# Kernel tuning notes

Hardware: AMD Instinct MI355X
Metric: run time of the kernel (lower is better)

## Reference

```python
import jax, jax.numpy as jnp
import numpy as np

NEG_SLOPE = 0.2  # leaky_relu negative slope (alpha)

def _glorot(key, shape):
    fan_in, fan_out = shape[0], shape[-1]
    lim = jnp.sqrt(6.0 / (fan_in + fan_out))
    return jax.random.uniform(key, shape, jnp.float32, -lim, lim)

def setup_inputs() -> dict:
    key = jax.random.key(0)
    ks = jax.random.split(key, 10)
    N, E, F_IN, HID, HEADS, NCLASS = 50000, 800000, 512, 32, 8, 32
    x = jax.random.normal(ks[0], (N, F_IN), jnp.float32)
    edge_index = jax.random.randint(ks[1], (2, E), 0, N, jnp.int64)
    # layer 1: heads=8, out per head = 32, concat -> 256
    W1 = _glorot(ks[2], (F_IN, HEADS * HID))
    att_src1 = _glorot(ks[3], (HEADS, HID))
    att_dst1 = _glorot(ks[4], (HEADS, HID))
    b1 = jnp.zeros((HEADS * HID,), jnp.float32)
    # layer 2: heads=1, out = nclass
    W2 = _glorot(ks[5], (HEADS * HID, NCLASS))
    att_src2 = _glorot(ks[6], (1, NCLASS))
    att_dst2 = _glorot(ks[7], (1, NCLASS))
    b2 = jnp.zeros((NCLASS,), jnp.float32)
    return {"x": x, "edge_index": edge_index, "W1": W1, "att_src1": att_src1,
            "att_dst1": att_dst1, "b1": b1, "W2": W2, "att_src2": att_src2,
            "att_dst2": att_dst2, "b2": b2}

def gat_conv(x, src, dst, W, a_src, a_dst, bias, num_nodes):
    """PyG GATConv (eval mode, self loops already appended to src/dst)."""
    H, C = a_src.shape
    h = (x @ W).reshape(num_nodes, H, C)                 # [N,H,C]
    score_src = jnp.einsum('nhc,hc->nh', h, a_src)       # [N,H]
    score_dst = jnp.einsum('nhc,hc->nh', h, a_dst)       # [N,H]
    e = jax.nn.leaky_relu(score_src[src] + score_dst[dst], NEG_SLOPE)  # [E,H]
    m = jax.ops.segment_max(e, dst, num_segments=num_nodes)           # [N,H]
    w = jnp.exp(e - m[dst])
    denom = jax.ops.segment_sum(w, dst, num_segments=num_nodes)       # [N,H]
    alpha = w / (denom[dst] + 1e-16)                                  # [E,H]
    out = jax.ops.segment_sum(alpha[:, :, None] * h[src], dst,
                              num_segments=num_nodes)                 # [N,H,C]
    return out.reshape(num_nodes, H * C) + bias

def reference(x, edge_index, W1, att_src1, att_dst1, b1, W2, att_src2, att_dst2, b2):
    N = x.shape[0]
    loops = jnp.arange(N, dtype=edge_index.dtype)
    src = jnp.concatenate([edge_index[0], loops])  # PyG add_self_loops=True
    dst = jnp.concatenate([edge_index[1], loops])
    h = jax.nn.elu(gat_conv(x, src, dst, W1, att_src1, att_dst1, b1, N))
    out = gat_conv(h, src, dst, W2, att_src2, att_dst2, b2, N)
    return out + 1e-06
```

## Files before the change

### kernel.cpp

```cpp
#include <hip/hip_runtime.h>
#include <math.h>

#define N_NODES 50000
#define N_EDGES 800000
#define E2 (N_EDGES + N_NODES)
#define F_IN 512
#define HEADS 8
#define HID 32
#define HC 256
#define NCLASS 32
#define NEG_SLOPE 0.2f
#define ELLW 64

typedef unsigned int uint;
typedef unsigned short ushort;
typedef __attribute__((ext_vector_type(8))) short bf16x8;
typedef __attribute__((ext_vector_type(4))) float f32x4;

#define GLOBAL_LOAD_LDS16(g, l) \
    __builtin_amdgcn_global_load_lds((const __attribute__((address_space(1))) void*)(g), \
                                     (__attribute__((address_space(3))) void*)(l), 16, 0, 0)

__device__ inline uint bf16_rne_bits(float f) {
    uint u = __float_as_uint(f);
    return (u + 0x7fffu + ((u >> 16) & 1u)) >> 16;
}
__device__ inline float bf2f(ushort u) { return __uint_as_float(((uint)u) << 16); }

#define W1_BLOCKS 512
#define W2_BLOCKS 32
#define FILL_BLOCKS ((E2 / 4 + 255) / 256)

__global__ void __launch_bounds__(256) prep_kernel(const float* __restrict__ W1,
        ushort* __restrict__ w1hi, ushort* __restrict__ w1lo,
        const float* __restrict__ W2, ushort* __restrict__ w2hi, ushort* __restrict__ w2lo,
        const int* __restrict__ ei, int* __restrict__ cursor, int* __restrict__ ell) {
    int b = blockIdx.x;
    if (b < W1_BLOCKS) {
        int t = b * 256 + threadIdx.x;
        int n = t >> 9, k = t & 511;
        float f = W1[k * 256 + n];
        uint h = bf16_rne_bits(f);
        float r = f - __uint_as_float(h << 16);
        w1hi[t] = (ushort)h;
        w1lo[t] = (ushort)bf16_rne_bits(r);
    } else if (b < W1_BLOCKS + W2_BLOCKS) {
        int t = (b - W1_BLOCKS) * 256 + threadIdx.x;
        int n = t >> 8, k = t & 255;
        float f = W2[k * 32 + n];
        uint h = bf16_rne_bits(f);
        float r = f - __uint_as_float(h << 16);
        w2hi[t] = (ushort)h;
        w2lo[t] = (ushort)bf16_rne_bits(r);
    } else {
        int e0 = ((b - W1_BLOCKS - W2_BLOCKS) * 256 + threadIdx.x) * 4;
        if (e0 < E2) {
            int src[4], dst[4];
            if (e0 < N_EDGES) {
                int4 s4 = *(const int4*)(ei + e0);
                int4 d4 = *(const int4*)(ei + N_EDGES + e0);
                src[0] = s4.x; src[1] = s4.y; src[2] = s4.z; src[3] = s4.w;
                dst[0] = d4.x; dst[1] = d4.y; dst[2] = d4.z; dst[3] = d4.w;
            } else {
                #pragma unroll
                for (int j = 0; j < 4; ++j) { src[j] = e0 + j - N_EDGES; dst[j] = src[j]; }
            }
            #pragma unroll
            for (int j = 0; j < 4; ++j) {
                int d = dst[j];
                int p = atomicAdd(&cursor[d], 1);
                ell[d * ELLW + p] = src[j];
            }
        }
    }
}

__global__ void __launch_bounds__(256) gemm1_mfma_kernel(const uint* __restrict__ xp,
        const ushort* __restrict__ bhi,
        const float* __restrict__ as1, const float* __restrict__ ad1,
        ushort* __restrict__ C, float* __restrict__ ssrc, float* __restrict__ sdst, int M) {
    __shared__ uint   As[128 * 32];
    __shared__ ushort Bh[128 * 32];
    const int tid = threadIdx.x, lane = tid & 63, wave = tid >> 6;

    const int NW = ((N_NODES + 127) / 128) * 2;
    const int orig = blockIdx.y * gridDim.x + blockIdx.x;
    const int xcd = orig & 7, idx = orig >> 3;
    const int q = NW >> 3, r = NW & 7;
    const int nid = (xcd < r ? xcd * (q + 1) : r * (q + 1) + (xcd - r) * q) + idx;
    const int bm = (nid >> 1) * 128, bn = (nid & 1) * 128;

    const uint* agp[4]; const uint* alp[4];
    #pragma unroll
    for (int s = 0; s < 4; ++s) {
        int t = wave * 4 + s;
        int p = t * 64 + lane;
        int row = p >> 3, cs = p & 7;
        int c = cs ^ (row & 7);
        int grow = bm + row; if (grow > M - 1) grow = M - 1;
        agp[s] = xp + ((size_t)grow * 512 + c * 4);
        alp[s] = &As[t * 256];
    }
    const ushort* bhgp[2]; const ushort* bhlp[2];
    #pragma unroll
    for (int s = 0; s < 2; ++s) {
        int t = wave * 2 + s;
        int p = t * 64 + lane;
        int row = p >> 2, qs = p & 3;
        int qq = qs ^ ((row >> 1) & 3);
        size_t go = (size_t)(bn + row) * 512 + qq * 8;
        bhgp[s] = bhi + go;
        bhlp[s] = &Bh[t * 512];
    }

    f32x4 acc[4][4] = {};
    const int wm = (wave >> 1) * 64, wn = (wave & 1) * 64;
    const int fm = lane & 15, quad = lane >> 4;

    for (int kk = 0; kk < 16; ++kk) {
        #pragma unroll
        for (int s = 0; s < 4; ++s) GLOBAL_LOAD_LDS16(agp[s], alp[s]);
        #pragma unroll
        for (int s = 0; s < 2; ++s) GLOBAL_LOAD_LDS16(bhgp[s], bhlp[s]);
        #pragma unroll
        for (int s = 0; s < 4; ++s) agp[s] += 32;
        #pragma unroll
        for (int s = 0; s < 2; ++s) bhgp[s] += 32;
        __syncthreads();

        bf16x8 ah[4], al[4], bh[4];
        #pragma unroll
        for (int i = 0; i < 4; ++i) {
            int row = wm + i * 16 + fm;
            int sw = row & 7;
            uint4 c0 = *(const uint4*)&As[row * 32 + (((2 * quad)     ^ sw) * 4)];
            uint4 c1 = *(const uint4*)&As[row * 32 + (((2 * quad + 1) ^ sw) * 4)];
            union { uint u[4]; bf16x8 v; } H, L;
            H.u[0] = __builtin_amdgcn_perm(c0.y, c0.x, 0x07060302u);
            H.u[1] = __builtin_amdgcn_perm(c0.w, c0.z, 0x07060302u);
            H.u[2] = __builtin_amdgcn_perm(c1.y, c1.x, 0x07060302u);
            H.u[3] = __builtin_amdgcn_perm(c1.w, c1.z, 0x07060302u);
            uint r0 = __float_as_uint(__uint_as_float(c0.x) - __uint_as_float(c0.x & 0xffff0000u));
            uint r1 = __float_as_uint(__uint_as_float(c0.y) - __uint_as_float(c0.y & 0xffff0000u));
            uint r2 = __float_as_uint(__uint_as_float(c0.z) - __uint_as_float(c0.z & 0xffff0000u));
            uint r3 = __float_as_uint(__uint_as_float(c0.w) - __uint_as_float(c0.w & 0xffff0000u));
            uint r4 = __float_as_uint(__uint_as_float(c1.x) - __uint_as_float(c1.x & 0xffff0000u));
            uint r5 = __float_as_uint(__uint_as_float(c1.y) - __uint_as_float(c1.y & 0xffff0000u));
            uint r6 = __float_as_uint(__uint_as_float(c1.z) - __uint_as_float(c1.z & 0xffff0000u));
            uint r7 = __float_as_uint(__uint_as_float(c1.w) - __uint_as_float(c1.w & 0xffff0000u));
            L.u[0] = __builtin_amdgcn_perm(r1, r0, 0x07060302u);
            L.u[1] = __builtin_amdgcn_perm(r3, r2, 0x07060302u);
            L.u[2] = __builtin_amdgcn_perm(r5, r4, 0x07060302u);
            L.u[3] = __builtin_amdgcn_perm(r7, r6, 0x07060302u);
            ah[i] = H.v; al[i] = L.v;
        }
        #pragma unroll
        for (int j = 0; j < 4; ++j) {
            int row = wn + j * 16 + fm;
            int qs = quad ^ ((row >> 1) & 3);
            bh[j] = *(const bf16x8*)&Bh[row * 32 + qs * 8];
        }
        #pragma unroll
        for (int i = 0; i < 4; ++i)
            #pragma unroll
            for (int j = 0; j < 4; ++j) {
                acc[i][j] = __builtin_amdgcn_mfma_f32_16x16x32_bf16(ah[i], bh[j], acc[i][j], 0, 0, 0);
                acc[i][j] = __builtin_amdgcn_mfma_f32_16x16x32_bf16(al[i], bh[j], acc[i][j], 0, 0, 0);
            }
        __syncthreads();
    }

    #pragma unroll
    for (int i = 0; i < 4; ++i) {
        int rb = bm + wm + i * 16 + quad * 4;
        #pragma unroll
        for (int j = 0; j < 4; ++j) {
            int col = bn + wn + j * 16 + fm;
            #pragma unroll
            for (int r2_ = 0; r2_ < 4; ++r2_) {
                int row = rb + r2_;
                if (row < M) C[(size_t)row * 256 + col] = (ushort)bf16_rne_bits(acc[i][j][r2_]);
            }
        }
    }

    const int head0 = (bn + wn) >> 5;
    const float asA0 = as1[head0 * 32 + fm],      asA1 = as1[head0 * 32 + 16 + fm];
    const float asB0 = as1[head0 * 32 + 32 + fm], asB1 = as1[head0 * 32 + 48 + fm];
    const float adA0 = ad1[head0 * 32 + fm],      adA1 = ad1[head0 * 32 + 16 + fm];
    const float adB0 = ad1[head0 * 32 + 32 + fm], adB1 = ad1[head0 * 32 + 48 + fm];
    #pragma unroll
    for (int i = 0; i < 4; ++i) {
        #pragma unroll
        for (int r2_ = 0; r2_ < 4; ++r2_) {
            int row = bm + wm + i * 16 + quad * 4 + r2_;
            float s1A = acc[i][0][r2_] * asA0 + acc[i][1][r2_] * asA1;
            float s1B = acc[i][2][r2_] * asB0 + acc[i][3][r2_] * asB1;
            float s2A = acc[i][0][r2_] * adA0 + acc[i][1][r2_] * adA1;
            float s2B = acc[i][2][r2_] * adB0 + acc[i][3][r2_] * adB1;
            #pragma unroll
            for (int off = 1; off < 16; off <<= 1) {
                s1A += __shfl_xor(s1A, off);
                s1B += __shfl_xor(s1B, off);
                s2A += __shfl_xor(s2A, off);
                s2B += __shfl_xor(s2B, off);
            }
            if (fm == 0 && row < M) {
                ssrc[(size_t)row * 8 + head0]     = s1A;
                ssrc[(size_t)row * 8 + head0 + 1] = s1B;
                sdst[(size_t)row * 8 + head0]     = s2A;
                sdst[(size_t)row * 8 + head0 + 1] = s2B;
            }
        }
    }
}

__global__ void __launch_bounds__(256) gemm2_mfma_kernel(const ushort* __restrict__ A,
        const ushort* __restrict__ bh_g, const ushort* __restrict__ bl_g,
        const float* __restrict__ as2, const float* __restrict__ ad2,
        ushort* __restrict__ C, float* __restrict__ ssrc, float* __restrict__ sdst, int M) {
    const int tid = threadIdx.x, lane = tid & 63, wave = tid >> 6;
    const int bm = blockIdx.x * 128;
    const int fm = lane & 15, quad = lane >> 4;
    const int wrow = wave * 32;

    int gr[2];
    #pragma unroll
    for (int i = 0; i < 2; ++i) {
        gr[i] = bm + wrow + i * 16 + fm;
        if (gr[i] > M - 1) gr[i] = M - 1;
    }

    f32x4 acc[2][2] = {};
    for (int kk = 0; kk < 8; ++kk) {
        bf16x8 a[2], bh[2], bl[2];
        #pragma unroll
        for (int i = 0; i < 2; ++i)
            a[i] = *(const bf16x8*)(A + (size_t)gr[i] * 256 + kk * 32 + quad * 8);
        #pragma unroll
        for (int j = 0; j < 2; ++j) {
            size_t off = (size_t)(j * 16 + fm) * 256 + kk * 32 + quad * 8;
            bh[j] = *(const bf16x8*)(bh_g + off);
            bl[j] = *(const bf16x8*)(bl_g + off);
        }
        #pragma unroll
        for (int i = 0; i < 2; ++i)
            #pragma unroll
            for (int j = 0; j < 2; ++j) {
                acc[i][j] = __builtin_amdgcn_mfma_f32_16x16x32_bf16(a[i], bh[j], acc[i][j], 0, 0, 0);
                acc[i][j] = __builtin_amdgcn_mfma_f32_16x16x32_bf16(a[i], bl[j], acc[i][j], 0, 0, 0);
            }
    }

    float a0 = as2[fm], a1 = as2[16 + fm];
    float d0 = ad2[fm], d1 = ad2[16 + fm];
    #pragma unroll
    for (int i = 0; i < 2; ++i) {
        #pragma unroll
        for (int r2_ = 0; r2_ < 4; ++r2_) {
            int rg = bm + wrow + i * 16 + quad * 4 + r2_;
            float v0 = acc[i][0][r2_], v1 = acc[i][1][r2_];
            float s1 = v0 * a0 + v1 * a1;
            float s2 = v0 * d0 + v1 * d1;
            #pragma unroll
            for (int off = 1; off < 16; off <<= 1) {
                s1 += __shfl_xor(s1, off);
                s2 += __shfl_xor(s2, off);
            }
            if (rg < M) {
                C[(size_t)rg * 32 + fm]      = (ushort)bf16_rne_bits(v0);
                C[(size_t)rg * 32 + 16 + fm] = (ushort)bf16_rne_bits(v1);
                if (fm == 0) { ssrc[rg] = s1; sdst[rg] = s2; }
            }
        }
    }
}

__global__ void __launch_bounds__(256) agg1_wave_kernel(const ushort* __restrict__ h,
        const float* __restrict__ ssrc, const float* __restrict__ sdst,
        const int* __restrict__ cnt, const int* __restrict__ ell,
        const float* __restrict__ bias, ushort* __restrict__ out) {
    const int wid = (blockIdx.x * blockDim.x + threadIdx.x) >> 6;
    if (wid >= N_NODES) return;
    const int lane = threadIdx.x & 63;
    const int hg = lane >> 3;
    const int hl = lane & 7;
    const int n = wid;
    const int beg = n * ELLW;
    const int end = beg + cnt[n];
    const float sdst_n = sdst[(size_t)n * HEADS + hg];

    float4 acc = make_float4(0.f, 0.f, 0.f, 0.f);
    float sw = 0.f;
    const ushort* hc = h + lane * 4;
    const int base = hg << 3;
    for (int e = beg; e < end; e += 16) {
        int ee0 = e + hl, ee1 = e + 8 + hl;
        int ei0 = ee0 < end ? ee0 : end - 1;
        int ei1 = ee1 < end ? ee1 : end - 1;
        int s0 = ell[ei0];
        int s1 = ell[ei1];
        float c0 = ssrc[(size_t)s0 * HEADS + hg] + sdst_n;
        float c1 = ssrc[(size_t)s1 * HEADS + hg] + sdst_n;
        c0 = c0 > 0.f ? c0 : NEG_SLOPE * c0;
        c1 = c1 > 0.f ? c1 : NEG_SLOPE * c1;
        float w0 = (ee0 < end) ? __expf(c0) : 0.f;
        float w1 = (ee1 < end) ? __expf(c1) : 0.f;
        float wj[16]; int sj[16];
        #pragma unroll
        for (int j = 0; j < 8; ++j) {
            wj[j]     = __shfl(w0, base + j);
            sj[j]     = __shfl(s0, base + j);
            wj[8 + j] = __shfl(w1, base + j);
            sj[8 + j] = __shfl(s1, base + j);
        }
        ushort4 v[16];
        #pragma unroll
        for (int j = 0; j < 16; ++j) v[j] = *(const ushort4*)(hc + (size_t)sj[j] * HC);
        #pragma unroll
        for (int j = 0; j < 16; ++j) {
            acc.x += wj[j] * bf2f(v[j].x);
            acc.y += wj[j] * bf2f(v[j].y);
            acc.z += wj[j] * bf2f(v[j].z);
            acc.w += wj[j] * bf2f(v[j].w);
            sw += wj[j];
        }
    }
    float inv = 1.f / (sw + 1e-16f);
    float4 bv = *(const float4*)(bias + lane * 4);
    float4 o;
    o.x = acc.x * inv + bv.x; o.y = acc.y * inv + bv.y;
    o.z = acc.z * inv + bv.z; o.w = acc.w * inv + bv.w;
    o.x = o.x > 0.f ? o.x : expm1f(o.x);
    o.y = o.y > 0.f ? o.y : expm1f(o.y);
    o.z = o.z > 0.f ? o.z : expm1f(o.z);
    o.w = o.w > 0.f ? o.w : expm1f(o.w);
    ushort4 ob;
    ob.x = (ushort)bf16_rne_bits(o.x);
    ob.y = (ushort)bf16_rne_bits(o.y);
    ob.z = (ushort)bf16_rne_bits(o.z);
    ob.w = (ushort)bf16_rne_bits(o.w);
    *(ushort4*)(out + (size_t)n * HC + lane * 4) = ob;
}

__global__ void __launch_bounds__(256) agg2_kernel(const ushort* __restrict__ h2,
        const float* __restrict__ ssrc, const float* __restrict__ sdst,
        const int* __restrict__ cnt, const int* __restrict__ ell,
        const float* __restrict__ bias, float* __restrict__ out) {
    const int n = blockIdx.x * 4 + (threadIdx.x >> 6);
    if (n >= N_NODES) return;
    const int beg = n * ELLW;
    const int end = beg + cnt[n];
    const int t = threadIdx.x & 63;
    const float sdst_n = sdst[n];

    const int slot = t >> 4, cp = t & 15;
    float a0 = 0.f, a1 = 0.f, sw = 0.f;
    for (int e = beg + slot; e < end; e += 4) {
        int src = ell[e];
        float sc = ssrc[src] + sdst_n;
        sc = sc > 0.f ? sc : NEG_SLOPE * sc;
        float w = __expf(sc);
        uint v = *(const uint*)(h2 + (size_t)src * NCLASS + cp * 2);
        a0 += w * __uint_as_float(v << 16);
        a1 += w * __uint_as_float(v & 0xffff0000u);
        sw += w;
    }
    a0 += __shfl_down(a0, 32); a1 += __shfl_down(a1, 32); sw += __shfl_down(sw, 32);
    a0 += __shfl_down(a0, 16); a1 += __shfl_down(a1, 16); sw += __shfl_down(sw, 16);
    if (t < 16) {
        float inv = 1.f / (sw + 1e-16f);
        float2 o;
        o.x = a0 * inv + bias[cp * 2]     + 1e-6f;
        o.y = a1 * inv + bias[cp * 2 + 1] + 1e-6f;
        *(float2*)(out + (size_t)n * NCLASS + cp * 2) = o;
    }
}

extern "C" void kernel_launch(void* const* d_in, const int* in_sizes, int n_in,
                              void* d_out, int out_size, void* d_ws, size_t ws_size,
                              hipStream_t stream) {
    const float* x        = (const float*)d_in[0];
    const int*   ei       = (const int*)  d_in[1];
    const float* W1       = (const float*)d_in[2];
    const float* att_src1 = (const float*)d_in[3];
    const float* att_dst1 = (const float*)d_in[4];
    const float* b1       = (const float*)d_in[5];
    const float* W2       = (const float*)d_in[6];
    const float* att_src2 = (const float*)d_in[7];
    const float* att_dst2 = (const float*)d_in[8];
    const float* b2       = (const float*)d_in[9];
    float* out = (float*)d_out;

    ushort* w1t_hi = (ushort*)d_ws;
    ushort* w1t_lo = w1t_hi + 256 * 512;
    ushort* w2t_hi = w1t_lo + 256 * 512;
    ushort* w2t_lo = w2t_hi + 32 * 256;
    ushort* h1b    = w2t_lo + 32 * 256;
    ushort* h2b    = h1b + (size_t)N_NODES * HC;
    ushort* out1b  = h2b + (size_t)N_NODES * NCLASS;
    float* ssrc1 = (float*)(out1b + (size_t)N_NODES * HC);
    float* sdst1 = ssrc1 + (size_t)N_NODES * HEADS;
    float* ssrc2 = sdst1 + (size_t)N_NODES * HEADS;
    float* sdst2 = ssrc2 + N_NODES;
    int* cursor  = (int*)(sdst2 + N_NODES);
    int* ell     = cursor + N_NODES;

    hipMemsetAsync(cursor, 0, N_NODES * sizeof(int), stream);
    prep_kernel<<<W1_BLOCKS + W2_BLOCKS + FILL_BLOCKS, 256, 0, stream>>>(
            W1, w1t_hi, w1t_lo, W2, w2t_hi, w2t_lo, ei, cursor, ell);

    {
        dim3 grid((N_NODES + 127) / 128, 2);
        gemm1_mfma_kernel<<<grid, 256, 0, stream>>>((const uint*)x, w1t_hi,
                att_src1, att_dst1, h1b, ssrc1, sdst1, N_NODES);
    }
    agg1_wave_kernel<<<(N_NODES + 3) / 4, 256, 0, stream>>>(h1b, ssrc1, sdst1, cursor, ell, b1, out1b);

    gemm2_mfma_kernel<<<(N_NODES + 127) / 128, 256, 0, stream>>>(out1b, w2t_hi, w2t_lo,
            att_src2, att_dst2, h2b, ssrc2, sdst2, N_NODES);
    agg2_kernel<<<(N_NODES + 3) / 4, 256, 0, stream>>>(h2b, ssrc2, sdst2, cursor, ell, b2, out);
}
```

Baseline: 362.6 us.

## Move ELL edge fill into gemm1 grid and drop bf16 low-part weight split

The edge-bucketing (ELL fill with atomics) moves out of the prep kernel and into extra blocks appended to the gemm1 launch, so the atomic scatter work can run alongside the first GEMM rather than before it. The prep kernel now only converts weights. The hi/lo bf16 split of W1/W2 is removed, and gemm2 drops the second MFMA pass over the low part, halving its MFMA work and B loads. The risk is lower precision in layer 2, and the GEMM blocks now contend with the atomic-heavy fill blocks.

```diff
diff --git a/kernel.cpp b/kernel.cpp
--- a/kernel.cpp
+++ b/kernel.cpp
@@ -29,31 +29,34 @@
 
 #define W1_BLOCKS 512
 #define W2_BLOCKS 32
-#define FILL_BLOCKS ((E2 / 4 + 255) / 256)
 
 __global__ void __launch_bounds__(256) prep_kernel(const float* __restrict__ W1,
-        ushort* __restrict__ w1hi, ushort* __restrict__ w1lo,
-        const float* __restrict__ W2, ushort* __restrict__ w2hi, ushort* __restrict__ w2lo,
-        const int* __restrict__ ei, int* __restrict__ cursor, int* __restrict__ ell) {
+        ushort* __restrict__ w1hi, const float* __restrict__ W2, ushort* __restrict__ w2hi) {
     int b = blockIdx.x;
     if (b < W1_BLOCKS) {
         int t = b * 256 + threadIdx.x;
         int n = t >> 9, k = t & 511;
-        float f = W1[k * 256 + n];
-        uint h = bf16_rne_bits(f);
-        float r = f - __uint_as_float(h << 16);
-        w1hi[t] = (ushort)h;
-        w1lo[t] = (ushort)bf16_rne_bits(r);
-    } else if (b < W1_BLOCKS + W2_BLOCKS) {
+        w1hi[t] = (ushort)bf16_rne_bits(W1[k * 256 + n]);
+    } else {
         int t = (b - W1_BLOCKS) * 256 + threadIdx.x;
         int n = t >> 8, k = t & 255;
-        float f = W2[k * 32 + n];
-        uint h = bf16_rne_bits(f);
-        float r = f - __uint_as_float(h << 16);
-        w2hi[t] = (ushort)h;
-        w2lo[t] = (ushort)bf16_rne_bits(r);
-    } else {
-        int e0 = ((b - W1_BLOCKS - W2_BLOCKS) * 256 + threadIdx.x) * 4;
+        w2hi[t] = (ushort)bf16_rne_bits(W2[k * 32 + n]);
+    }
+}
+
+#define NWG1 (((N_NODES + 127) / 128) * 2)
+#define FILL_BLOCKS ((E2 / 4 + 255) / 256)
+
+__global__ void __launch_bounds__(256) gemm1_mfma_kernel(const uint* __restrict__ xp,
+        const ushort* __restrict__ bhi,
+        const float* __restrict__ as1, const float* __restrict__ ad1,
+        ushort* __restrict__ C, float* __restrict__ ssrc, float* __restrict__ sdst, int M,
+        const int* __restrict__ ei, int* __restrict__ cursor, int* __restrict__ ell) {
+    __shared__ uint   As[128 * 32];
+    __shared__ ushort Bh[128 * 32];
+
+    if (blockIdx.x >= NWG1) {
+        int e0 = ((blockIdx.x - NWG1) * 256 + threadIdx.x) * 4;
         if (e0 < E2) {
             int src[4], dst[4];
             if (e0 < N_EDGES) {
@@ -72,21 +75,14 @@
                 ell[d * ELLW + p] = src[j];
             }
         }
-    }
-}
-
-__global__ void __launch_bounds__(256) gemm1_mfma_kernel(const uint* __restrict__ xp,
-        const ushort* __restrict__ bhi,
-        const float* __restrict__ as1, const float* __restrict__ ad1,
-        ushort* __restrict__ C, float* __restrict__ ssrc, float* __restrict__ sdst, int M) {
-    __shared__ uint   As[128 * 32];
-    __shared__ ushort Bh[128 * 32];
+        return;
+    }
+
     const int tid = threadIdx.x, lane = tid & 63, wave = tid >> 6;
 
-    const int NW = ((N_NODES + 127) / 128) * 2;
-    const int orig = blockIdx.y * gridDim.x + blockIdx.x;
+    const int orig = blockIdx.x;
     const int xcd = orig & 7, idx = orig >> 3;
-    const int q = NW >> 3, r = NW & 7;
+    const int q = NWG1 >> 3, r = NWG1 & 7;
     const int nid = (xcd < r ? xcd * (q + 1) : r * (q + 1) + (xcd - r) * q) + idx;
     const int bm = (nid >> 1) * 128, bn = (nid & 1) * 128;
 
@@ -216,7 +212,7 @@
 }
 
 __global__ void __launch_bounds__(256) gemm2_mfma_kernel(const ushort* __restrict__ A,
-        const ushort* __restrict__ bh_g, const ushort* __restrict__ bl_g,
+        const ushort* __restrict__ bh_g,
         const float* __restrict__ as2, const float* __restrict__ ad2,
         ushort* __restrict__ C, float* __restrict__ ssrc, float* __restrict__ sdst, int M) {
     const int tid = threadIdx.x, lane = tid & 63, wave = tid >> 6;
@@ -233,7 +229,7 @@
 
     f32x4 acc[2][2] = {};
     for (int kk = 0; kk < 8; ++kk) {
-        bf16x8 a[2], bh[2], bl[2];
+        bf16x8 a[2], bh[2];
         #pragma unroll
         for (int i = 0; i < 2; ++i)
             a[i] = *(const bf16x8*)(A + (size_t)gr[i] * 256 + kk * 32 + quad * 8);
@@ -241,15 +237,12 @@
         for (int j = 0; j < 2; ++j) {
             size_t off = (size_t)(j * 16 + fm) * 256 + kk * 32 + quad * 8;
             bh[j] = *(const bf16x8*)(bh_g + off);
-            bl[j] = *(const bf16x8*)(bl_g + off);
         }
         #pragma unroll
         for (int i = 0; i < 2; ++i)
             #pragma unroll
-            for (int j = 0; j < 2; ++j) {
+            for (int j = 0; j < 2; ++j)
                 acc[i][j] = __builtin_amdgcn_mfma_f32_16x16x32_bf16(a[i], bh[j], acc[i][j], 0, 0, 0);
-                acc[i][j] = __builtin_amdgcn_mfma_f32_16x16x32_bf16(a[i], bl[j], acc[i][j], 0, 0, 0);
-            }
     }
 
     float a0 = as2[fm], a1 = as2[16 + fm];
@@ -393,10 +386,8 @@
     float* out = (float*)d_out;
 
     ushort* w1t_hi = (ushort*)d_ws;
-    ushort* w1t_lo = w1t_hi + 256 * 512;
-    ushort* w2t_hi = w1t_lo + 256 * 512;
-    ushort* w2t_lo = w2t_hi + 32 * 256;
-    ushort* h1b    = w2t_lo + 32 * 256;
+    ushort* w2t_hi = w1t_hi + 256 * 512;
+    ushort* h1b    = w2t_hi + 32 * 256;
     ushort* h2b    = h1b + (size_t)N_NODES * HC;
     ushort* out1b  = h2b + (size_t)N_NODES * NCLASS;
     float* ssrc1 = (float*)(out1b + (size_t)N_NODES * HC);
@@ -407,17 +398,13 @@
     int* ell     = cursor + N_NODES;
 
     hipMemsetAsync(cursor, 0, N_NODES * sizeof(int), stream);
-    prep_kernel<<<W1_BLOCKS + W2_BLOCKS + FILL_BLOCKS, 256, 0, stream>>>(
-            W1, w1t_hi, w1t_lo, W2, w2t_hi, w2t_lo, ei, cursor, ell);
-
-    {
-        dim3 grid((N_NODES + 127) / 128, 2);
-        gemm1_mfma_kernel<<<grid, 256, 0, stream>>>((const uint*)x, w1t_hi,
-                att_src1, att_dst1, h1b, ssrc1, sdst1, N_NODES);
-    }
+    prep_kernel<<<W1_BLOCKS + W2_BLOCKS, 256, 0, stream>>>(W1, w1t_hi, W2, w2t_hi);
+
+    gemm1_mfma_kernel<<<NWG1 + FILL_BLOCKS, 256, 0, stream>>>((const uint*)x, w1t_hi,
+            att_src1, att_dst1, h1b, ssrc1, sdst1, N_NODES, ei, cursor, ell);
     agg1_wave_kernel<<<(N_NODES + 3) / 4, 256, 0, stream>>>(h1b, ssrc1, sdst1, cursor, ell, b1, out1b);
 
-    gemm2_mfma_kernel<<<(N_NODES + 127) / 128, 256, 0, stream>>>(out1b, w2t_hi, w2t_lo,
+    gemm2_mfma_kernel<<<(N_NODES + 127) / 128, 256, 0, stream>>>(out1b, w2t_hi,
             att_src2, att_dst2, h2b, ssrc2, sdst2, N_NODES);
     agg2_kernel<<<(N_NODES + 3) / 4, 256, 0, stream>>>(h2b, ssrc2, sdst2, cursor, ell, b2, out);
 }
```

Result: faster. 328.3 us (-9.5%).
